# Kernel optimization log

Measured on AMD Instinct MI355X. Metric: run time of the kernel, lower is better.

Reference implementation:

```python
import jax, jax.numpy as jnp
from jax import lax
import numpy as np

A = 2048          # number of agents
H = 128           # hidden_dim
G = 8             # grid_size
NB = 32.0         # neighbourhood_size
CELL = 2.0 * NB / G


def setup_inputs() -> dict:
    key = jax.random.key(0)
    k1, k2, k3 = jax.random.split(key, 3)
    hidden = jax.random.normal(k1, (A, H), dtype=jnp.float32)
    # positions spread wider than the neighbourhood so bins are exercised
    pos = jax.random.uniform(k2, (A, 2), dtype=jnp.float32, minval=-48.0, maxval=48.0)
    mask = jnp.ones((A,), dtype=bool)
    W = jax.random.normal(k3, (H, G * G * H), dtype=jnp.float32) * (1.0 / np.sqrt(G * G * H))
    b = jnp.zeros((H,), dtype=jnp.float32)
    return {"hidden": hidden, "pos": pos, "mask": mask, "W": W, "b": b}


def reference(hidden, pos, mask, W, b):
    a, h = hidden.shape
    # rel[i, j] = pos[j] - pos[i]  (matches `rel = pos - pos[i]` indexed at j)
    rel = pos[None, :, :] - pos[:, None, :]          # [A, A, 2]
    rx, ry = rel[..., 0], rel[..., 1]
    in_range = (jnp.abs(rx) < NB) & (jnp.abs(ry) < NB)  # also False for NaN rel
    col = jnp.clip(jnp.floor((rx + NB) / CELL).astype(jnp.int32), 0, G - 1)
    row = jnp.clip(jnp.floor((ry + NB) / CELL).astype(jnp.int32), 0, G - 1)
    bins = row * G + col                              # [A, A] in [0, G*G)
    not_self = ~jnp.eye(a, dtype=bool)
    valid = in_range & not_self & mask[None, :]       # [A, A]

    # grid[i, bcell, :] = sum over j with bins[i,j]==bcell of hidden[j]
    def scan_body(_, bcell):
        Mb = (valid & (bins == bcell)).astype(hidden.dtype)   # [A, A]
        return None, Mb @ hidden                              # [A, H]

    _, grid = lax.scan(scan_body, None, jnp.arange(G * G))    # [G*G, A, H]
    grid = jnp.transpose(grid, (1, 0, 2)).reshape(a, G * G * h)
    pooled = grid @ W.T + b                                   # [A, H]

    valid_i = mask & ~jnp.isnan(pos).any(axis=-1)
    return jnp.where(valid_i[:, None], pooled, jnp.zeros_like(pooled))
```

## Files before the change

kernel.cpp:

```cpp
#include <hip/hip_runtime.h>
#include <hip/hip_bf16.h>
#include <stdint.h>


typedef __attribute__((ext_vector_type(4))) float f32x4;
typedef __attribute__((ext_vector_type(8))) short short8;

#define O_HB   0u
#define O_WB   1048576u
#define O_GRID 3145728u
#define O_PART 36700160u

__device__ __forceinline__ void gl_lds16(const void* g, void* l) {
  __builtin_amdgcn_global_load_lds((const __attribute__((address_space(1))) void*)g,
                                   (__attribute__((address_space(3))) void*)l, 16, 0, 0);
}

__device__ __forceinline__ float bf_lo(uint32_t w) {
  union { uint32_t u; float f; } v{w << 16}; return v.f;
}
__device__ __forceinline__ float bf_hi(uint32_t w) {
  union { uint32_t u; float f; } v{w & 0xffff0000u}; return v.f;
}
__device__ __forceinline__ uint32_t pack_bf2(float x, float y) {
  __hip_bfloat16 bx = __float2bfloat16(x), by = __float2bfloat16(y);
  return ((uint32_t)(*(unsigned short*)&by) << 16) | (*(unsigned short*)&bx);
}

__global__ __launch_bounds__(256) void sp_prep(const float* __restrict__ hidden,
                                               const float* __restrict__ W,
                                               __hip_bfloat16* __restrict__ hb,
                                               __hip_bfloat16* __restrict__ wb) {
  int idx = blockIdx.x * 256 + threadIdx.x;
  const int HID4 = (2049 * 128) / 4;
  const int W4   = (128 * 8192) / 4;
  if (idx < HID4) {
    int e = idx * 4;
    float4 v = make_float4(0.f, 0.f, 0.f, 0.f);
    if (e < 2048 * 128) v = *reinterpret_cast<const float4*>(hidden + e);
    ushort4 pk;
    pk.x = (ushort)(pack_bf2(v.x, v.x) & 0xffffu);
    pk.y = (ushort)(pack_bf2(v.y, v.y) & 0xffffu);
    pk.z = (ushort)(pack_bf2(v.z, v.z) & 0xffffu);
    pk.w = (ushort)(pack_bf2(v.w, v.w) & 0xffffu);
    *reinterpret_cast<ushort4*>(hb + e) = pk;
  } else if (idx < HID4 + W4) {
    int e = (idx - HID4) * 4;
    float4 v = *reinterpret_cast<const float4*>(W + e);
    ushort4 pk;
    pk.x = (ushort)(pack_bf2(v.x, v.x) & 0xffffu);
    pk.y = (ushort)(pack_bf2(v.y, v.y) & 0xffffu);
    pk.z = (ushort)(pack_bf2(v.z, v.z) & 0xffffu);
    pk.w = (ushort)(pack_bf2(v.w, v.w) & 0xffffu);
    *reinterpret_cast<ushort4*>(wb + e) = pk;
  }
}

__global__ __launch_bounds__(256) void sp_build(const float* __restrict__ pos,
                                                const int* __restrict__ mask,
                                                const __hip_bfloat16* __restrict__ hb,
                                                __hip_bfloat16* __restrict__ grid) {
  __shared__ __align__(8) uint16_t list[2304];
  __shared__ int hist[4][64];
  __shared__ int cur[4][64];
  __shared__ int offs[65];
  int t = threadIdx.x;
  int wv = t >> 6;
  int i = blockIdx.x;
  float pxi = pos[2 * i], pyi = pos[2 * i + 1];
  reinterpret_cast<int*>(hist)[t] = 0;
  __syncthreads();
  const float2* pos2 = reinterpret_cast<const float2*>(pos);
  int bins[8];
  #pragma unroll
  for (int jj = 0; jj < 8; ++jj) {
    int j = t + jj * 256;
    float2 pj = pos2[j];
    float rx = pj.x - pxi, ry = pj.y - pyi;
    bool ok = (fabsf(rx) < 32.f) && (fabsf(ry) < 32.f) && (j != i) && (mask[j] != 0);
    int b = -1;
    if (ok) {
      int col = (int)floorf((rx + 32.f) * 0.125f);
      int row = (int)floorf((ry + 32.f) * 0.125f);
      b = row * 8 + col;
      atomicAdd(&hist[wv][b], 1);
    }
    bins[jj] = b;
  }
  #pragma unroll
  for (int q = 0; q < 9; ++q) {
    int k = t + q * 256;
    if (k < 2304) list[k] = 2048;
  }
  __syncthreads();
  if (t < 64) {
    int h0 = hist[0][t], h1 = hist[1][t], h2 = hist[2][t], h3 = hist[3][t];
    int tot = h0 + h1 + h2 + h3;
    int padded = (tot + 3) & ~3;
    int x = padded;
    #pragma unroll
    for (int d = 1; d < 64; d <<= 1) {
      int y = __shfl_up(x, d);
      if (t >= d) x += y;
    }
    offs[t + 1] = x;
    int base = x - padded;
    cur[0][t] = base;
    cur[1][t] = base + h0;
    cur[2][t] = base + h0 + h1;
    cur[3][t] = base + h0 + h1 + h2;
    if (t == 0) offs[0] = 0;
  }
  __syncthreads();
  #pragma unroll
  for (int jj = 0; jj < 8; ++jj) {
    int j = t + jj * 256;
    int b = bins[jj];
    if (b >= 0) { int k = atomicAdd(&cur[wv][b], 1); list[k] = (uint16_t)j; }
  }
  __syncthreads();
  int l = t & 63;
  int hi5 = l >> 5;
  int lq = l & 31;
  const uint2* hb2 = reinterpret_cast<const uint2*>(hb);
  for (int c = wv; c < 64; c += 4) {
    int s0 = offs[c], e0 = offs[c + 1];
    float a0 = 0.f, a1 = 0.f, a2 = 0.f, a3 = 0.f;
    float b0 = 0.f, b1 = 0.f, b2 = 0.f, b3 = 0.f;
    for (int k = s0; k + 4 <= e0; k += 4) {
      int jA = (int)list[k + hi5];
      int jB = (int)list[k + 2 + hi5];
      uint2 wA = hb2[jA * 32 + lq];
      uint2 wB = hb2[jB * 32 + lq];
      a0 += bf_lo(wA.x); a1 += bf_hi(wA.x);
      a2 += bf_lo(wA.y); a3 += bf_hi(wA.y);
      b0 += bf_lo(wB.x); b1 += bf_hi(wB.x);
      b2 += bf_lo(wB.y); b3 += bf_hi(wB.y);
    }
    float c0 = a0 + b0, c1 = a1 + b1, c2 = a2 + b2, c3 = a3 + b3;
    c0 += __shfl_xor(c0, 32);
    c1 += __shfl_xor(c1, 32);
    c2 += __shfl_xor(c2, 32);
    c3 += __shfl_xor(c3, 32);
    if (l < 32) {
      uint2 pk;
      pk.x = pack_bf2(c0, c1);
      pk.y = pack_bf2(c2, c3);
      *reinterpret_cast<uint2*>(
          reinterpret_cast<char*>(grid) + ((size_t)((i << 6) + c) * 256 + (size_t)lq * 8)) = pk;
    }
  }
}

__global__ __launch_bounds__(256) void sp_gemm(const __hip_bfloat16* __restrict__ Ag,
                                               const __hip_bfloat16* __restrict__ Wb,
                                               float* __restrict__ part) {
  __shared__ __align__(16) char Asm[8192];
  __shared__ __align__(16) char Bsm[16384];
  int t = threadIdx.x;
  int lane = t & 63;
  int w = t >> 6;
  int wm = w >> 1, wn = w & 1;
  int bx = blockIdx.x;
  int mt = bx & 31;
  int sp = bx >> 5;
  int i0 = mt * 64;
  long kbase = (long)sp * 512 * 2;
  const char* Agc = (const char*)Ag;
  const char* Wbc = (const char*)Wb;
  f32x4 acc[2][4] = {};
  for (int st = 0; st < 8; ++st) {
    long kb = kbase + st * 128;
    #pragma unroll
    for (int q = 0; q < 2; ++q) {
      int o = (q * 256 + t) * 16;
      int r = o >> 7;
      int sc = (o & 127) ^ ((r & 7) << 4);
      gl_lds16(Agc + (long)(i0 + r) * 16384 + kb + sc, Asm + o);
    }
    #pragma unroll
    for (int q = 0; q < 4; ++q) {
      int o = (q * 256 + t) * 16;
      int r = o >> 7;
      int sc = (o & 127) ^ ((r & 7) << 4);
      gl_lds16(Wbc + (long)r * 16384 + kb + sc, Bsm + o);
    }
    __syncthreads();
    short8 af[2][2], bfr[4][2];
    #pragma unroll
    for (int fr = 0; fr < 2; ++fr)
      #pragma unroll
      for (int ks = 0; ks < 2; ++ks) {
        int r = wm * 32 + fr * 16 + (lane & 15);
        int g = ks * 4 + (lane >> 4);
        int byt = r * 128 + ((g ^ (r & 7)) << 4);
        af[fr][ks] = *reinterpret_cast<const short8*>(Asm + byt);
      }
    #pragma unroll
    for (int fc = 0; fc < 4; ++fc)
      #pragma unroll
      for (int ks = 0; ks < 2; ++ks) {
        int n = wn * 64 + fc * 16 + (lane & 15);
        int g = ks * 4 + (lane >> 4);
        int byt = n * 128 + ((g ^ (n & 7)) << 4);
        bfr[fc][ks] = *reinterpret_cast<const short8*>(Bsm + byt);
      }
    #pragma unroll
    for (int fr = 0; fr < 2; ++fr)
      #pragma unroll
      for (int fc = 0; fc < 4; ++fc)
        #pragma unroll
        for (int ks = 0; ks < 2; ++ks)
          acc[fr][fc] = __builtin_amdgcn_mfma_f32_16x16x32_bf16(af[fr][ks], bfr[fc][ks],
                                                                acc[fr][fc], 0, 0, 0);
    __syncthreads();
  }
  float* p = part + (long)sp * 262144;
  #pragma unroll
  for (int fr = 0; fr < 2; ++fr)
    #pragma unroll
    for (int fc = 0; fc < 4; ++fc)
      #pragma unroll
      for (int r4 = 0; r4 < 4; ++r4) {
        int ii = i0 + wm * 32 + fr * 16 + (lane >> 4) * 4 + r4;
        int nn = wn * 64 + fc * 16 + (lane & 15);
        p[(long)ii * 128 + nn] = acc[fr][fc][r4];
      }
}

__global__ __launch_bounds__(256) void sp_reduce(const float* __restrict__ part,
                                                 const float* __restrict__ bias,
                                                 const float* __restrict__ pos,
                                                 const int* __restrict__ mask,
                                                 float* __restrict__ out) {
  int g = blockIdx.x * 256 + threadIdx.x;
  int i = g >> 7, n = g & 127;
  float acc = bias[n];
  #pragma unroll
  for (int s = 0; s < 16; ++s) acc += part[(long)s * 262144 + g];
  float px = pos[2 * i], py = pos[2 * i + 1];
  bool vi = (mask[i] != 0) && (px == px) && (py == py);
  out[g] = vi ? acc : 0.f;
}

extern "C" void kernel_launch(void* const* d_in, const int* in_sizes, int n_in,
                              void* d_out, int out_size, void* d_ws, size_t ws_size,
                              hipStream_t stream) {
  const float* hidden  = (const float*)d_in[0];
  const float* pos     = (const float*)d_in[1];
  const int*   mask    = (const int*)d_in[2];
  const float* W       = (const float*)d_in[3];
  const float* bias    = (const float*)d_in[4];
  char* ws = (char*)d_ws;
  __hip_bfloat16* hb   = (__hip_bfloat16*)(ws + O_HB);
  __hip_bfloat16* wb   = (__hip_bfloat16*)(ws + O_WB);
  __hip_bfloat16* grid = (__hip_bfloat16*)(ws + O_GRID);
  float* part          = (float*)(ws + O_PART);
  float* out           = (float*)d_out;

  sp_prep<<<1281, 256, 0, stream>>>(hidden, W, hb, wb);
  sp_build<<<2048, 256, 0, stream>>>(pos, mask, hb, grid);
  sp_gemm<<<512, 256, 0, stream>>>(grid, wb, part);
  sp_reduce<<<1024, 256, 0, stream>>>(part, bias, pos, mask, out);
}
```

Baseline: 68.56 us.

## Pipeline neighbour gathers with byte-offset lists and fold mask into positions

The neighbour list now holds 32-bit byte offsets instead of 16-bit indices, with bins padded to multiples of 8. Each wave reads four offsets with one vector LDS load and issues four row gathers per step. The gathers are software-pipelined so the next batch of loads is in flight while the current one is accumulated. The prep kernel also folds the mask into a NaN-marked position array, so the build kernel no longer loads the mask per neighbour. The cost is more LDS for the list, extra padding gathers of the zero row, and a posm buffer that shares its workspace offset with the partial-sum buffer.

```diff
diff --git a/kernel.cpp b/kernel.cpp
--- a/kernel.cpp
+++ b/kernel.cpp
@@ -10,6 +10,7 @@
 #define O_WB   1048576u
 #define O_GRID 3145728u
 #define O_PART 36700160u
+#define O_POSM 36700160u
 
 __device__ __forceinline__ void gl_lds16(const void* g, void* l) {
   __builtin_amdgcn_global_load_lds((const __attribute__((address_space(1))) void*)g,
@@ -29,8 +30,11 @@
 
 __global__ __launch_bounds__(256) void sp_prep(const float* __restrict__ hidden,
                                                const float* __restrict__ W,
+                                               const float* __restrict__ pos,
+                                               const int* __restrict__ mask,
                                                __hip_bfloat16* __restrict__ hb,
-                                               __hip_bfloat16* __restrict__ wb) {
+                                               __hip_bfloat16* __restrict__ wb,
+                                               float2* __restrict__ posm) {
   int idx = blockIdx.x * 256 + threadIdx.x;
   const int HID4 = (2049 * 128) / 4;
   const int W4   = (128 * 8192) / 4;
@@ -53,14 +57,25 @@
     pk.z = (ushort)(pack_bf2(v.z, v.z) & 0xffffu);
     pk.w = (ushort)(pack_bf2(v.w, v.w) & 0xffffu);
     *reinterpret_cast<ushort4*>(wb + e) = pk;
+  } else {
+    int j = idx - (HID4 + W4);
+    if (j < 2048) {
+      float2 p = reinterpret_cast<const float2*>(pos)[j];
+      union { uint32_t u; float f; } qn{0x7fc00000u};
+      float2 o;
+      bool m = (mask[j] != 0);
+      o.x = m ? p.x : qn.f;
+      o.y = m ? p.y : qn.f;
+      posm[j] = o;
+    }
   }
 }
 
 __global__ __launch_bounds__(256) void sp_build(const float* __restrict__ pos,
-                                                const int* __restrict__ mask,
+                                                const float2* __restrict__ posm,
                                                 const __hip_bfloat16* __restrict__ hb,
                                                 __hip_bfloat16* __restrict__ grid) {
-  __shared__ __align__(8) uint16_t list[2304];
+  __shared__ __align__(16) uint32_t list32[2560];
   __shared__ int hist[4][64];
   __shared__ int cur[4][64];
   __shared__ int offs[65];
@@ -70,14 +85,13 @@
   float pxi = pos[2 * i], pyi = pos[2 * i + 1];
   reinterpret_cast<int*>(hist)[t] = 0;
   __syncthreads();
-  const float2* pos2 = reinterpret_cast<const float2*>(pos);
   int bins[8];
   #pragma unroll
   for (int jj = 0; jj < 8; ++jj) {
     int j = t + jj * 256;
-    float2 pj = pos2[j];
+    float2 pj = posm[j];
     float rx = pj.x - pxi, ry = pj.y - pyi;
-    bool ok = (fabsf(rx) < 32.f) && (fabsf(ry) < 32.f) && (j != i) && (mask[j] != 0);
+    bool ok = (fabsf(rx) < 32.f) && (fabsf(ry) < 32.f) && (j != i);
     int b = -1;
     if (ok) {
       int col = (int)floorf((rx + 32.f) * 0.125f);
@@ -88,15 +102,15 @@
     bins[jj] = b;
   }
   #pragma unroll
-  for (int q = 0; q < 9; ++q) {
+  for (int q = 0; q < 10; ++q) {
     int k = t + q * 256;
-    if (k < 2304) list[k] = 2048;
+    if (k < 2560) list32[k] = (2048u << 8);
   }
   __syncthreads();
   if (t < 64) {
     int h0 = hist[0][t], h1 = hist[1][t], h2 = hist[2][t], h3 = hist[3][t];
     int tot = h0 + h1 + h2 + h3;
-    int padded = (tot + 3) & ~3;
+    int padded = (tot + 7) & ~7;
     int x = padded;
     #pragma unroll
     for (int d = 1; d < 64; d <<= 1) {
@@ -116,26 +130,40 @@
   for (int jj = 0; jj < 8; ++jj) {
     int j = t + jj * 256;
     int b = bins[jj];
-    if (b >= 0) { int k = atomicAdd(&cur[wv][b], 1); list[k] = (uint16_t)j; }
+    if (b >= 0) { int k = atomicAdd(&cur[wv][b], 1); list32[k] = ((uint32_t)j << 8); }
   }
   __syncthreads();
   int l = t & 63;
-  int hi5 = l >> 5;
   int lq = l & 31;
-  const uint2* hb2 = reinterpret_cast<const uint2*>(hb);
+  int dsh = (l >> 5) << 2;
+  int lqoff = lq * 8;
+  const char* hbB = reinterpret_cast<const char*>(hb);
   for (int c = wv; c < 64; c += 4) {
     int s0 = offs[c], e0 = offs[c + 1];
     float a0 = 0.f, a1 = 0.f, a2 = 0.f, a3 = 0.f;
     float b0 = 0.f, b1 = 0.f, b2 = 0.f, b3 = 0.f;
-    for (int k = s0; k + 4 <= e0; k += 4) {
-      int jA = (int)list[k + hi5];
-      int jB = (int)list[k + 2 + hi5];
-      uint2 wA = hb2[jA * 32 + lq];
-      uint2 wB = hb2[jB * 32 + lq];
-      a0 += bf_lo(wA.x); a1 += bf_hi(wA.x);
-      a2 += bf_lo(wA.y); a3 += bf_hi(wA.y);
-      b0 += bf_lo(wB.x); b1 += bf_hi(wB.x);
-      b2 += bf_lo(wB.y); b3 += bf_hi(wB.y);
+    if (s0 < e0) {
+      uint4 js = *reinterpret_cast<const uint4*>(&list32[s0 + dsh]);
+      uint2 r0 = *reinterpret_cast<const uint2*>(hbB + js.x + lqoff);
+      uint2 r1 = *reinterpret_cast<const uint2*>(hbB + js.y + lqoff);
+      uint2 r2 = *reinterpret_cast<const uint2*>(hbB + js.z + lqoff);
+      uint2 r3 = *reinterpret_cast<const uint2*>(hbB + js.w + lqoff);
+      for (int k = s0 + 8; k < e0; k += 8) {
+        uint4 jn = *reinterpret_cast<const uint4*>(&list32[k + dsh]);
+        uint2 n0 = *reinterpret_cast<const uint2*>(hbB + jn.x + lqoff);
+        uint2 n1 = *reinterpret_cast<const uint2*>(hbB + jn.y + lqoff);
+        uint2 n2 = *reinterpret_cast<const uint2*>(hbB + jn.z + lqoff);
+        uint2 n3 = *reinterpret_cast<const uint2*>(hbB + jn.w + lqoff);
+        a0 += bf_lo(r0.x); a1 += bf_hi(r0.x); a2 += bf_lo(r0.y); a3 += bf_hi(r0.y);
+        b0 += bf_lo(r1.x); b1 += bf_hi(r1.x); b2 += bf_lo(r1.y); b3 += bf_hi(r1.y);
+        a0 += bf_lo(r2.x); a1 += bf_hi(r2.x); a2 += bf_lo(r2.y); a3 += bf_hi(r2.y);
+        b0 += bf_lo(r3.x); b1 += bf_hi(r3.x); b2 += bf_lo(r3.y); b3 += bf_hi(r3.y);
+        r0 = n0; r1 = n1; r2 = n2; r3 = n3;
+      }
+      a0 += bf_lo(r0.x); a1 += bf_hi(r0.x); a2 += bf_lo(r0.y); a3 += bf_hi(r0.y);
+      b0 += bf_lo(r1.x); b1 += bf_hi(r1.x); b2 += bf_lo(r1.y); b3 += bf_hi(r1.y);
+      a0 += bf_lo(r2.x); a1 += bf_hi(r2.x); a2 += bf_lo(r2.y); a3 += bf_hi(r2.y);
+      b0 += bf_lo(r3.x); b1 += bf_hi(r3.x); b2 += bf_lo(r3.y); b3 += bf_hi(r3.y);
     }
     float c0 = a0 + b0, c1 = a1 + b1, c2 = a2 + b2, c3 = a3 + b3;
     c0 += __shfl_xor(c0, 32);
@@ -256,10 +284,11 @@
   __hip_bfloat16* wb   = (__hip_bfloat16*)(ws + O_WB);
   __hip_bfloat16* grid = (__hip_bfloat16*)(ws + O_GRID);
   float* part          = (float*)(ws + O_PART);
+  float2* posm         = (float2*)(ws + O_POSM);
   float* out           = (float*)d_out;
 
-  sp_prep<<<1281, 256, 0, stream>>>(hidden, W, hb, wb);
-  sp_build<<<2048, 256, 0, stream>>>(pos, mask, hb, grid);
+  sp_prep<<<1289, 256, 0, stream>>>(hidden, W, pos, mask, hb, wb, posm);
+  sp_build<<<2048, 256, 0, stream>>>(pos, posm, hb, grid);
   sp_gemm<<<512, 256, 0, stream>>>(grid, wb, part);
   sp_reduce<<<1024, 256, 0, stream>>>(part, bias, pos, mask, out);
 }
```

New measurement: 67.65 us. About the same (-1.3%).
